# Kernel optimization log

Measured on AMD Instinct MI355X. Metric: run time of the kernel, lower is better.

The kernel has to match this reference:

```python
import jax, jax.numpy as jnp
import numpy as np

EPS = 1e-14
RHO = 8.0


def _normalize(x):
    return x / jnp.linalg.norm(x, axis=-1, keepdims=True)


def setup_inputs() -> dict:
    key = jax.random.key(0)
    ks = jax.random.split(key, 12)
    B, D = 4096, 1024
    f = lambda k: _normalize(jax.random.normal(k, (B, D), dtype=jnp.float32))
    pos = lambda k: jax.random.uniform(k, (B, 1), dtype=jnp.float32, minval=0.1, maxval=1.0)
    return {
        "im_feat": f(ks[0]),
        "tt_feat": f(ks[1]),
        "rim_feat": f(ks[2]),
        "rtt_feat": f(ks[3]),
        "remote_u_im": pos(ks[4]),
        "remote_u_tt": pos(ks[5]),
        "loss1_im": pos(ks[6]),
        "loss1_tt": pos(ks[7]),
        "u_im": pos(ks[8]),
        "u_tt": pos(ks[9]),
        "logit_scale": 10.0 * jnp.ones((1,), dtype=jnp.float32),
        "offset": 0,
    }


def _pairwise_loss(rim, rtt, im, tt, logit_scale, offset):
    # features1 = remote, features2 = local (as in forward(): pairwise_loss(remote_features, features, ...))
    sim_image = rim @ tt.T                                  # [B1, B2]
    sim_text = rtt @ im.T                                   # [B1, B2]
    diag_sim = jnp.sum(rim * rtt, axis=-1, keepdims=True)   # [B1, 1]
    exp_im = jnp.exp((sim_image - diag_sim) * logit_scale)
    exp_tt = jnp.exp((sim_text - diag_sim) * logit_scale)
    B1, B2 = sim_image.shape
    # mask zeros the shifted diagonal: equivalent to subtracting the diagonal entry from the row sum
    cols = (jnp.arange(B1) + offset)[:, None]               # [B1, 1]
    rw_sum = B2 - 1 if B1 <= B2 else B2 * (B1 - 1) / B1
    loss_im = (jnp.sum(exp_im, axis=-1, keepdims=True)
               - jnp.take_along_axis(exp_im, cols, axis=1)) / rw_sum
    loss_tt = (jnp.sum(exp_tt, axis=-1, keepdims=True)
               - jnp.take_along_axis(exp_tt, cols, axis=1)) / rw_sum
    return loss_im, loss_tt


def reference(im_feat, tt_feat, rim_feat, rtt_feat, remote_u_im, remote_u_tt,
              loss1_im, loss1_tt, u_im, u_tt, logit_scale, offset):
    loss2_im, loss2_tt = _pairwise_loss(rim_feat, rtt_feat, im_feat, tt_feat, logit_scale, offset)
    pg1 = loss1_im / (u_im + EPS) + loss1_tt / (u_tt + EPS)
    pg2 = loss2_im / (remote_u_im + EPS) + loss2_tt / (remote_u_tt + EPS)
    loss = (jnp.mean(pg1) + jnp.mean(pg2)) / 2
    # multiply_tau branch
    ls = logit_scale[0]
    loss = loss / jax.lax.stop_gradient(ls)
    loss = loss + RHO / ls
    loss = loss + jnp.mean(jnp.log(u_im) + jnp.log(u_tt)) / 2 / ls
    return loss
```

## Files before the change

kernel.cpp:

```cpp
#include <hip/hip_runtime.h>
#include <hip/hip_bf16.h>

#define EPSF 1e-14f
#define RHOF 8.0f

typedef __attribute__((ext_vector_type(4))) float f32x4;
typedef __attribute__((ext_vector_type(2))) unsigned long long u64x2;

#define AS_GLOBAL __attribute__((address_space(1)))
#define AS_LDS    __attribute__((address_space(3)))


__global__ __launch_bounds__(256) void prep_fp8(
    const float* __restrict__ im,  const float* __restrict__ tt,
    const float* __restrict__ rim, const float* __restrict__ rtt,
    unsigned char* __restrict__ bIm,  unsigned char* __restrict__ bTt,
    unsigned char* __restrict__ bRim, unsigned char* __restrict__ bRtt,
    float* __restrict__ S_im, float* __restrict__ S_tt,
    float* __restrict__ diag, float* __restrict__ red,
    int D, int spm )
{
    __shared__ unsigned char L[8 * 1024];
    const int b = blockIdx.x;
    const int tid = threadIdx.x;
    const int nConv = 4 * spm;
    if (b < nConv) {
        int mIdx = b / spm;
        int slab = b - mIdx * spm;
        const float* src = (mIdx == 0) ? rim : (mIdx == 1) ? tt
                          : (mIdx == 2) ? rtt : im;
        unsigned char* dst = (mIdx == 0) ? bRim : (mIdx == 1) ? bTt
                            : (mIdx == 2) ? bRtt : bIm;
        const float* srow = src + (size_t)slab * 8 * D;
        const int n4 = (8 * D) >> 2;
        for (int idx = tid; idx < n4; idx += 256) {
            float4 v = *(const float4*)(srow + idx * 4);
            int pk = __builtin_amdgcn_cvt_pk_fp8_f32(v.x, v.y, 0, false);
            pk     = __builtin_amdgcn_cvt_pk_fp8_f32(v.z, v.w, pk, true);
            *(int*)&L[idx * 4] = pk;
        }
        __syncthreads();
        const int kTiles = D >> 7;
        const int rb = (slab * 8) >> 7;
        const int r0loc = (slab * 8) & 127;
        for (int g = tid; g < (D >> 1); g += 256) {
            int kb  = g >> 6;
            int rem = g & 63;
            int rl  = rem >> 3;
            int h   = rem & 7;
            int r   = slab * 8 + rl;
            int m   = r & 15;
            int g0  = (2 * h) ^ m;
            int g1  = (2 * h + 1) ^ m;
            const unsigned char* lb = &L[rl * D + kb * 128];
            u64x2 o;
            o.x = *(const unsigned long long*)(lb + g0 * 8);
            o.y = *(const unsigned long long*)(lb + g1 * 8);
            char* outp = (char*)dst
                       + ((size_t)(rb * kTiles + kb) * 1024
                          + (size_t)(r0loc + rl) * 8 + h) * 16;
            *(u64x2*)outp = o;
        }
    } else {
        int db = b - nConv;
        if (db == 0 && tid < 8) red[tid] = 0.f;
        if (tid < 4) { S_im[db * 4 + tid] = 0.f; S_tt[db * 4 + tid] = 0.f; }
        int row  = db * 4 + (tid >> 6);
        int lane = tid & 63;
        const float* a = rim + (size_t)row * D;
        const float* c = rtt + (size_t)row * D;
        float s = 0.f;
        for (int k = lane * 4; k < D; k += 256) {
            float4 av = *(const float4*)(a + k);
            float4 cv = *(const float4*)(c + k);
            s += av.x * cv.x + av.y * cv.y + av.z * cv.z + av.w * cv.w;
        }
        #pragma unroll
        for (int m2 = 1; m2 < 64; m2 <<= 1) s += __shfl_xor(s, m2, 64);
        if (lane == 0) diag[row] = s;
    }
}

__global__ __launch_bounds__(256) void gemm_expsum(
    const unsigned char* __restrict__ A0, const unsigned char* __restrict__ B0,
    float* __restrict__ S0,
    const unsigned char* __restrict__ A1, const unsigned char* __restrict__ B1,
    float* __restrict__ S1,
    const float* __restrict__ logit_scale, const int* __restrict__ offset,
    int Bn, int D)
{
    const int z = blockIdx.z;
    const unsigned char* A = z ? A1 : A0;
    const unsigned char* B = z ? B1 : B0;
    float* S = z ? S1 : S0;

    __shared__ unsigned char As[16384];
    __shared__ unsigned char Bs[16384];

    const int tid  = threadIdx.x;
    const int wave = tid >> 6;
    const int lane = tid & 63;
    const int lo   = lane & 15;
    const int qd   = lane >> 4;
    const int m0   = (wave >> 1) * 64;
    const int n0   = (wave & 1) * 64;
    int soff[4];
    #pragma unroll
    for (int s = 0; s < 4; ++s) soff[s] = ((4 * s + qd) ^ lo) * 8;

    const int kTiles = D >> 7;
    const unsigned char* Atile = A + (size_t)blockIdx.y * kTiles * 16384;
    const unsigned char* Btile = B + (size_t)blockIdx.x * kTiles * 16384;

    f32x4 acc[4][4];
    #pragma unroll
    for (int i = 0; i < 4; ++i)
        #pragma unroll
        for (int j = 0; j < 4; ++j)
            acc[i][j] = (f32x4){0.f, 0.f, 0.f, 0.f};

    for (int kb = 0; kb < kTiles; ++kb) {
        #pragma unroll
        for (int j = 0; j < 4; ++j) {
            int goff = (j * 256 + tid) * 16;
            int loff = j * 4096 + wave * 1024;
            __builtin_amdgcn_global_load_lds(
                (const AS_GLOBAL unsigned int*)(Atile + goff),
                (AS_LDS unsigned int*)&As[loff], 16, 0, 0);
            __builtin_amdgcn_global_load_lds(
                (const AS_GLOBAL unsigned int*)(Btile + goff),
                (AS_LDS unsigned int*)&Bs[loff], 16, 0, 0);
        }
        __syncthreads();

        #pragma unroll
        for (int s = 0; s < 4; ++s) {
            long af[4], bq[4];
            #pragma unroll
            for (int t = 0; t < 4; ++t) {
                af[t] = *(const long*)&As[(m0 + 16 * t + lo) * 128 + soff[s]];
                bq[t] = *(const long*)&Bs[(n0 + 16 * t + lo) * 128 + soff[s]];
            }
            #pragma unroll
            for (int ti = 0; ti < 4; ++ti)
                #pragma unroll
                for (int tj = 0; tj < 4; ++tj)
                    acc[ti][tj] = __builtin_amdgcn_mfma_f32_16x16x32_fp8_fp8(
                        af[ti], bq[tj], acc[ti][tj], 0, 0, 0);
        }
        __syncthreads();

        Atile += 16384;
        Btile += 16384;
    }

    const float ls = logit_scale[0];
    const int offs = offset[0];
    const int rowBase = blockIdx.y * 128;
    const int colBase = blockIdx.x * 128;
    #pragma unroll
    for (int ti = 0; ti < 4; ++ti) {
        #pragma unroll
        for (int r = 0; r < 4; ++r) {
            int gi = rowBase + m0 + 16 * ti + 4 * qd + r;
            float rs = 0.f;
            #pragma unroll
            for (int tj = 0; tj < 4; ++tj) {
                int gj = colBase + n0 + 16 * tj + lo;
                float e = __expf(ls * acc[ti][tj][r]);
                if (gj == gi + offs) e = 0.f;
                rs += e;
            }
            #pragma unroll
            for (int m = 1; m < 16; m <<= 1) rs += __shfl_xor(rs, m, 64);
            if (lo == 0) atomicAdd(&S[gi], rs);
        }
    }
}

__global__ __launch_bounds__(256) void final_kernel(
    const float* __restrict__ S_im, const float* __restrict__ S_tt,
    const float* __restrict__ diag,
    const float* __restrict__ ru_im, const float* __restrict__ ru_tt,
    const float* __restrict__ l1_im, const float* __restrict__ l1_tt,
    const float* __restrict__ u_im,  const float* __restrict__ u_tt,
    const float* __restrict__ logit_scale, float* __restrict__ red,
    float* __restrict__ out, int Bn)
{
    const float ls = logit_scale[0];
    const float inv_rw = 1.0f / (float)(Bn - 1);
    const int gid = blockIdx.x * 256 + threadIdx.x;
    float pg = 0.f, lg = 0.f;
    for (int i = gid; i < Bn; i += 8 * 256) {
        float p1 = l1_im[i] / (u_im[i] + EPSF) + l1_tt[i] / (u_tt[i] + EPSF);
        float dd = expf(-ls * diag[i]);
        float p2 = dd * S_im[i] * inv_rw / (ru_im[i] + EPSF)
                 + dd * S_tt[i] * inv_rw / (ru_tt[i] + EPSF);
        pg += p1 + p2;
        lg += logf(u_im[i]) + logf(u_tt[i]);
    }
    __shared__ float sp[256], sl[256];
    sp[threadIdx.x] = pg; sl[threadIdx.x] = lg;
    __syncthreads();
    for (int s = 128; s > 0; s >>= 1) {
        if (threadIdx.x < s) { sp[threadIdx.x] += sp[threadIdx.x + s];
                               sl[threadIdx.x] += sl[threadIdx.x + s]; }
        __syncthreads();
    }
    if (threadIdx.x == 0) {
        atomicAdd(&red[0], sp[0]);
        atomicAdd(&red[1], sl[0]);
        __threadfence();
        int t = atomicAdd((int*)&red[2], 1);
        if (t == gridDim.x - 1) {
            float pgSum = atomicAdd(&red[0], 0.f);
            float lgSum = atomicAdd(&red[1], 0.f);
            float loss = ((pgSum / (float)Bn) * 0.5f) / ls
                       + RHOF / ls
                       + (lgSum / (float)Bn) * 0.5f / ls;
            out[0] = loss;
        }
    }
}

extern "C" void kernel_launch(void* const* d_in, const int* in_sizes, int n_in,
                              void* d_out, int out_size, void* d_ws, size_t ws_size,
                              hipStream_t stream) {
    const float* im    = (const float*)d_in[0];
    const float* tt    = (const float*)d_in[1];
    const float* rim   = (const float*)d_in[2];
    const float* rtt   = (const float*)d_in[3];
    const float* ru_im = (const float*)d_in[4];
    const float* ru_tt = (const float*)d_in[5];
    const float* l1_im = (const float*)d_in[6];
    const float* l1_tt = (const float*)d_in[7];
    const float* u_im  = (const float*)d_in[8];
    const float* u_tt  = (const float*)d_in[9];
    const float* lsc   = (const float*)d_in[10];
    const int*   offs  = (const int*)d_in[11];

    const int Bn = in_sizes[4];
    const int D  = in_sizes[0] / Bn;
    const int spm = Bn / 8;

    char* base = (char*)d_ws;
    float* S_im = (float*)base;
    float* S_tt = S_im + Bn;
    float* diag = S_tt + Bn;
    float* red  = diag + Bn;
    const size_t headBytes = (((size_t)(3 * Bn + 8) * sizeof(float)) + 255) & ~(size_t)255;
    const size_t matBytes  = (size_t)Bn * D;
    unsigned char* buf0 = (unsigned char*)(base + headBytes);
    unsigned char* bRim = buf0;
    unsigned char* bTt  = buf0 + matBytes;
    unsigned char* bRtt = buf0 + 2 * matBytes;
    unsigned char* bIm  = buf0 + 3 * matBytes;

    prep_fp8<<<4 * spm + Bn / 4, 256, 0, stream>>>(
        im, tt, rim, rtt, bIm, bTt, bRim, bRtt, S_im, S_tt, diag, red, D, spm);

    dim3 ggrid(Bn / 128, Bn / 128, 2);
    gemm_expsum<<<ggrid, 256, 0, stream>>>(bRim, bTt, S_im, bRtt, bIm, S_tt,
                                           lsc, offs, Bn, D);

    final_kernel<<<8, 256, 0, stream>>>(S_im, S_tt, diag, ru_im, ru_tt,
                                        l1_im, l1_tt, u_im, u_tt, lsc,
                                        red, (float*)d_out, Bn);
}
```

Before: 202.1 us.

## Use 16x16x128 scaled FP8 MFMA with double-buffered LDS and new swizzle

Replaces the four 16x16x32 fp8 MFMAs per k-step with a single 16x16x128 scaled MFMA (unit scales), which takes 32-byte operand fragments loaded as two 16-byte LDS reads. The prep kernel's swizzle is changed to 16-byte granules to match the new fragment layout. The GEMM also double-buffers the LDS tiles so the next k-tile's global-to-LDS copy is issued before computing on the current one. The aim is fewer MFMA and LDS instructions and overlap of loads with compute, at the cost of doubled LDS use (64 KB), which may lower occupancy.

After: 186.4 us. 1.08x faster.

```diff
diff --git a/kernel.cpp b/kernel.cpp
--- a/kernel.cpp
+++ b/kernel.cpp
@@ -5,6 +5,7 @@
 #define RHOF 8.0f
 
 typedef __attribute__((ext_vector_type(4))) float f32x4;
+typedef __attribute__((ext_vector_type(8))) int   i32x8;
 typedef __attribute__((ext_vector_type(2))) unsigned long long u64x2;
 
 #define AS_GLOBAL __attribute__((address_space(1)))
@@ -47,18 +48,14 @@
             int kb  = g >> 6;
             int rem = g & 63;
             int rl  = rem >> 3;
-            int h   = rem & 7;
+            int p   = rem & 7;
             int r   = slab * 8 + rl;
-            int m   = r & 15;
-            int g0  = (2 * h) ^ m;
-            int g1  = (2 * h + 1) ^ m;
-            const unsigned char* lb = &L[rl * D + kb * 128];
-            u64x2 o;
-            o.x = *(const unsigned long long*)(lb + g0 * 8);
-            o.y = *(const unsigned long long*)(lb + g1 * 8);
+            int c   = p ^ (r & 7);
+            const unsigned char* lb = &L[rl * D + kb * 128 + c * 16];
+            u64x2 o = *(const u64x2*)lb;
             char* outp = (char*)dst
                        + ((size_t)(rb * kTiles + kb) * 1024
-                          + (size_t)(r0loc + rl) * 8 + h) * 16;
+                          + (size_t)(r0loc + rl) * 8 + p) * 16;
             *(u64x2*)outp = o;
         }
     } else {
@@ -94,8 +91,8 @@
     const unsigned char* B = z ? B1 : B0;
     float* S = z ? S1 : S0;
 
-    __shared__ unsigned char As[16384];
-    __shared__ unsigned char Bs[16384];
+    __shared__ unsigned char As[2][16384];
+    __shared__ unsigned char Bs[2][16384];
 
     const int tid  = threadIdx.x;
     const int wave = tid >> 6;
@@ -104,49 +101,66 @@
     const int qd   = lane >> 4;
     const int m0   = (wave >> 1) * 64;
     const int n0   = (wave & 1) * 64;
-    int soff[4];
-    #pragma unroll
-    for (int s = 0; s < 4; ++s) soff[s] = ((4 * s + qd) ^ lo) * 8;
+    const int s0   = (2 * qd) ^ (lo & 7);
+    const int offA = s0 * 16;
+    const int offB = (s0 ^ 1) * 16;
 
     const int kTiles = D >> 7;
     const unsigned char* Atile = A + (size_t)blockIdx.y * kTiles * 16384;
     const unsigned char* Btile = B + (size_t)blockIdx.x * kTiles * 16384;
 
-    f32x4 acc[4][4];
-    #pragma unroll
-    for (int i = 0; i < 4; ++i)
-        #pragma unroll
-        for (int j = 0; j < 4; ++j)
-            acc[i][j] = (f32x4){0.f, 0.f, 0.f, 0.f};
-
-    for (int kb = 0; kb < kTiles; ++kb) {
+    auto stage = [&](int buf, const unsigned char* At, const unsigned char* Bt) {
         #pragma unroll
         for (int j = 0; j < 4; ++j) {
             int goff = (j * 256 + tid) * 16;
             int loff = j * 4096 + wave * 1024;
             __builtin_amdgcn_global_load_lds(
-                (const AS_GLOBAL unsigned int*)(Atile + goff),
-                (AS_LDS unsigned int*)&As[loff], 16, 0, 0);
+                (const AS_GLOBAL unsigned int*)(At + goff),
+                (AS_LDS unsigned int*)&As[buf][loff], 16, 0, 0);
             __builtin_amdgcn_global_load_lds(
-                (const AS_GLOBAL unsigned int*)(Btile + goff),
-                (AS_LDS unsigned int*)&Bs[loff], 16, 0, 0);
-        }
-        __syncthreads();
-
-        #pragma unroll
-        for (int s = 0; s < 4; ++s) {
-            long af[4], bq[4];
+                (const AS_GLOBAL unsigned int*)(Bt + goff),
+                (AS_LDS unsigned int*)&Bs[buf][loff], 16, 0, 0);
+        }
+    };
+
+    f32x4 acc[4][4];
+    #pragma unroll
+    for (int i = 0; i < 4; ++i)
+        #pragma unroll
+        for (int j = 0; j < 4; ++j)
+            acc[i][j] = (f32x4){0.f, 0.f, 0.f, 0.f};
+
+    stage(0, Atile, Btile);
+    __syncthreads();
+
+    for (int kb = 0; kb < kTiles; ++kb) {
+        const int cur = kb & 1;
+        if (kb + 1 < kTiles)
+            stage(1 - cur, Atile + 16384, Btile + 16384);
+
+        i32x8 bq[4];
+        #pragma unroll
+        for (int t = 0; t < 4; ++t) {
+            int rn = (n0 + 16 * t + lo) * 128;
+            union { int4 h[2]; i32x8 v; } u;
+            u.h[0] = *(const int4*)&Bs[cur][rn + offA];
+            u.h[1] = *(const int4*)&Bs[cur][rn + offB];
+            bq[t] = u.v;
+        }
+        #pragma unroll
+        for (int ti = 0; ti < 4; ++ti) {
+            int ra = (m0 + 16 * ti + lo) * 128;
+            union { int4 h[2]; i32x8 v; } u;
+            u.h[0] = *(const int4*)&As[cur][ra + offA];
+            u.h[1] = *(const int4*)&As[cur][ra + offB];
+            i32x8 af = u.v;
             #pragma unroll
-            for (int t = 0; t < 4; ++t) {
-                af[t] = *(const long*)&As[(m0 + 16 * t + lo) * 128 + soff[s]];
-                bq[t] = *(const long*)&Bs[(n0 + 16 * t + lo) * 128 + soff[s]];
-            }
-            #pragma unroll
-            for (int ti = 0; ti < 4; ++ti)
-                #pragma unroll
-                for (int tj = 0; tj < 4; ++tj)
-                    acc[ti][tj] = __builtin_amdgcn_mfma_f32_16x16x32_fp8_fp8(
-                        af[ti], bq[tj], acc[ti][tj], 0, 0, 0);
+            for (int tj = 0; tj < 4; ++tj)
+                acc[ti][tj] = __builtin_amdgcn_mfma_scale_f32_16x16x128_f8f6f4(
+                    af, bq[tj], acc[ti][tj],
+                    0, 0,
+                    0, 127,
+                    0, 127);
         }
         __syncthreads();
 
```
